# Kernel optimization log

Measured on AMD Instinct MI355X. Metric: run time of the kernel, lower is better.

Reference implementation:

```python
import jax, jax.numpy as jnp
import numpy as np

EPS = 1e-12

def sage_layer(x, src, dst, Wl, Wr, b, n_nodes):
    # mean aggregation of source-node features into destination nodes
    msgs = x[src]                                            # [E, F] gather
    s = jax.ops.segment_sum(msgs, dst, num_segments=n_nodes)  # [N, F]
    cnt = jax.ops.segment_sum(jnp.ones((src.shape[0],), x.dtype), dst, num_segments=n_nodes)
    agg = s / jnp.maximum(cnt, 1.0)[:, None]                 # mean; 0 for isolated nodes
    out = agg @ Wl + b + x @ Wr                              # lin_l(agg) + lin_r(x_i)
    norm = jnp.linalg.norm(out, axis=-1, keepdims=True)      # normalize=True -> L2 norm
    return out / jnp.maximum(norm, EPS)


def setup_inputs() -> dict:
    key = jax.random.key(0)
    ks = jax.random.split(key, 8)
    N, E, F = 100000, 1200000, 64
    H1, H2, OUT = 64, 32, 10  # hidden_channels//2, hidden_channels//4, output_dim
    x = jax.random.normal(ks[0], (N, F), dtype=jnp.float32)
    edge_index = jax.random.randint(ks[1], (2, E), 0, N, dtype=jnp.int64)
    def glorot(k, fin, fout):
        lim = np.sqrt(6.0 / (fin + fout)).astype(np.float32)
        return jax.random.uniform(k, (fin, fout), jnp.float32, -lim, lim)
    return {
        "x": x,
        "edge_index": edge_index,
        "W1l": glorot(ks[2], F, H1), "W1r": glorot(ks[3], F, H1), "b1": jnp.zeros((H1,), jnp.float32),
        "W2l": glorot(ks[4], H1, H2), "W2r": glorot(ks[5], H1, H2), "b2": jnp.zeros((H2,), jnp.float32),
        "W3l": glorot(ks[6], H2, OUT), "W3r": glorot(ks[7], H2, OUT), "b3": jnp.zeros((OUT,), jnp.float32),
    }


def reference(x, edge_index, W1l, W1r, b1, W2l, W2r, b2, W3l, W3r, b3):
    n = x.shape[0]
    src, dst = edge_index[0], edge_index[1]
    h = jax.nn.relu(sage_layer(x, src, dst, W1l, W1r, b1, n))
    h = jax.nn.relu(sage_layer(h, src, dst, W2l, W2r, b2, n))
    h = sage_layer(h, src, dst, W3l, W3r, b3, n)
    return jax.nn.log_softmax(h, axis=1)
```

## Files before the change

kernel.cpp:

```cpp
#include <hip/hip_runtime.h>
#include <math.h>


typedef __attribute__((ext_vector_type(8))) short short8;
typedef __attribute__((ext_vector_type(4))) float floatx4;

__device__ __forceinline__ unsigned short f2bf(float f) {
    unsigned u = __float_as_uint(f);
    u += 0x7fffu + ((u >> 16) & 1u);
    return (unsigned short)(u >> 16);
}
__device__ __forceinline__ float blo(unsigned u) { return __uint_as_float(u << 16); }
__device__ __forceinline__ float bhi(unsigned u) { return __uint_as_float(u & 0xffff0000u); }


__global__ __launch_bounds__(256) void hist_kernel(
        const int* __restrict__ ei, int* __restrict__ bh, int E, int NB, int NBKT) {
    __shared__ int lh[256];
    const int tid = threadIdx.x, blk = blockIdx.x;
    if (tid < NBKT) lh[tid] = 0;
    __syncthreads();
    const int base = blk << 12;
#pragma unroll
    for (int i = 0; i < 16; ++i) {
        const int e = base + (i << 8) + tid;
        if (e < E) atomicAdd(&lh[((unsigned)ei[E + e]) >> 9], 1);
    }
    __syncthreads();
    if (tid < NBKT) bh[tid * NB + blk] = lh[tid];
}

__global__ __launch_bounds__(256) void bscan_kernel(
        const int* __restrict__ bh, int* __restrict__ offs, int* __restrict__ btot,
        int NB, int NBKT) {
    const int lane = threadIdx.x & 63;
    const int w = blockIdx.x * 4 + (threadIdx.x >> 6);
    if (w >= NBKT) return;
    int running = 0;
    for (int base = 0; base < NB; base += 64) {
        const int j = base + lane;
        const int v = (j < NB) ? bh[w * NB + j] : 0;
        int incl = v;
#pragma unroll
        for (int off = 1; off < 64; off <<= 1) {
            const int t = __shfl_up(incl, off);
            if (lane >= off) incl += t;
        }
        if (j < NB) offs[w * NB + j] = running + incl - v;
        running += __shfl(incl, 63);
    }
    if (lane == 0) btot[w] = running;
}

__global__ __launch_bounds__(64) void bucketbase_kernel(
        const int* __restrict__ btot, int* __restrict__ bucket_base, int NBKT) {
    const int lane = threadIdx.x;
    int running = 0;
    for (int base = 0; base < NBKT; base += 64) {
        const int j = base + lane;
        const int v = (j < NBKT) ? btot[j] : 0;
        int incl = v;
#pragma unroll
        for (int off = 1; off < 64; off <<= 1) {
            const int t = __shfl_up(incl, off);
            if (lane >= off) incl += t;
        }
        if (j < NBKT) bucket_base[j] = running + incl - v;
        running += __shfl(incl, 63);
    }
    if (lane == 0) bucket_base[NBKT] = running;
}

__global__ __launch_bounds__(256) void scatter_kernel(
        const int* __restrict__ ei, const int* __restrict__ offs,
        const int* __restrict__ bucket_base, unsigned* __restrict__ ebuf,
        int E, int NB, int NBKT) {
    __shared__ int lcur[256];
    const int tid = threadIdx.x, blk = blockIdx.x;
    if (tid < NBKT) lcur[tid] = bucket_base[tid] + offs[tid * NB + blk];
    __syncthreads();
    const int base = blk << 12;
#pragma unroll
    for (int i = 0; i < 16; ++i) {
        const int e = base + (i << 8) + tid;
        if (e < E) {
            const int s = ei[e];
            const unsigned d = (unsigned)ei[E + e];
            const int p = atomicAdd(&lcur[d >> 9], 1);
            ebuf[p] = ((d & 511u) << 17) | (unsigned)s;
        }
    }
}

__global__ __launch_bounds__(512) void bucket_csr_kernel(
        const unsigned* __restrict__ ebuf, const int* __restrict__ bucket_base,
        int* __restrict__ rowptr, int* __restrict__ deg, int* __restrict__ col,
        int N) {
    __shared__ int ldeg[512];
    __shared__ int buf[512];
    __shared__ int lcur[512];
    const int b = blockIdx.x, tid = threadIdx.x;
    const int segbase = bucket_base[b];
    const int L = bucket_base[b + 1] - segbase;
    ldeg[tid] = 0;
    __syncthreads();
    for (int i = tid; i < L; i += 512) atomicAdd(&ldeg[ebuf[segbase + i] >> 17], 1);
    __syncthreads();
    buf[tid] = ldeg[tid];
    __syncthreads();
    for (int off = 1; off < 512; off <<= 1) {
        const int t = (tid >= off) ? buf[tid - off] : 0;
        __syncthreads();
        buf[tid] += t;
        __syncthreads();
    }
    const int excl = buf[tid] - ldeg[tid];
    const int node = (b << 9) + tid;
    if (node < N) { rowptr[node] = segbase + excl; deg[node] = ldeg[tid]; }
    lcur[tid] = excl;
    __syncthreads();
    for (int i = tid; i < L; i += 512) {
        const unsigned p = ebuf[segbase + i];
        const int pos = atomicAdd(&lcur[p >> 17], 1);
        col[segbase + pos] = (int)(p & 0x1FFFFu);
    }
}

template <int K, int F_OUT, int PAD, bool AFP32>
__global__ __launch_bounds__(256) void transform_kernel(
        const void* __restrict__ Ain, const float* __restrict__ Wl,
        const float* __restrict__ Wr, const float* __restrict__ b,
        unsigned short* __restrict__ yl, float* __restrict__ yr, int n) {
    constexpr int KSTEP = K / 32;
    constexpr int NT = PAD / 16;
    const int lane = threadIdx.x & 63;
    const int wid = (blockIdx.x * blockDim.x + threadIdx.x) >> 6;
    const int ntiles = (n + 15) >> 4;
    if (wid >= ntiles) return;
    const int nl = lane & 15, q = lane >> 4;

    short8 Bl[NT][KSTEP], Br[NT][KSTEP];
    float biasv[NT];
#pragma unroll
    for (int t = 0; t < NT; ++t) {
        const int ncol = t * 16 + nl;
        biasv[t] = (ncol < F_OUT) ? b[ncol] : 0.f;
#pragma unroll
        for (int ks = 0; ks < KSTEP; ++ks) {
#pragma unroll
            for (int j = 0; j < 8; ++j) {
                const int k = ks * 32 + q * 8 + j;
                Bl[t][ks][j] = (ncol < F_OUT) ? (short)f2bf(Wl[k * F_OUT + ncol]) : (short)0;
                Br[t][ks][j] = (ncol < F_OUT) ? (short)f2bf(Wr[k * F_OUT + ncol]) : (short)0;
            }
        }
    }

    const int m0 = wid * 16;
    int m = m0 + nl; if (m >= n) m = n - 1;

    short8 a[KSTEP];
#pragma unroll
    for (int ks = 0; ks < KSTEP; ++ks) {
        if (AFP32) {
            const float* p = (const float*)Ain + (size_t)m * K + ks * 32 + q * 8;
#pragma unroll
            for (int j = 0; j < 8; ++j) a[ks][j] = (short)f2bf(p[j]);
        } else {
            union { uint4 u; short8 s; } cvt;
            cvt.u = *(const uint4*)((const unsigned short*)Ain + (size_t)m * K + ks * 32 + q * 8);
            a[ks] = cvt.s;
        }
    }

    floatx4 accl[NT], accr[NT];
#pragma unroll
    for (int t = 0; t < NT; ++t) { accl[t] = {0.f,0.f,0.f,0.f}; accr[t] = {0.f,0.f,0.f,0.f}; }
#pragma unroll
    for (int ks = 0; ks < KSTEP; ++ks) {
#pragma unroll
        for (int t = 0; t < NT; ++t) {
            accl[t] = __builtin_amdgcn_mfma_f32_16x16x32_bf16(a[ks], Bl[t][ks], accl[t], 0, 0, 0);
            accr[t] = __builtin_amdgcn_mfma_f32_16x16x32_bf16(a[ks], Br[t][ks], accr[t], 0, 0, 0);
        }
    }

#pragma unroll
    for (int t = 0; t < NT; ++t) {
        const int ncol = t * 16 + nl;
#pragma unroll
        for (int r = 0; r < 4; ++r) {
            const int node = m0 + q * 4 + r;
            if (node < n) {
                yl[(size_t)node * PAD + ncol] = f2bf(accl[t][r]);
                yr[(size_t)node * PAD + ncol] = accr[t][r] + biasv[t];
            }
        }
    }
}

template <int F, int ACT>
__global__ __launch_bounds__(256) void agg_kernel(
        const unsigned short* __restrict__ yl, const float* __restrict__ yr,
        const int* __restrict__ rowptr, const int* __restrict__ degv,
        const int* __restrict__ col,
        unsigned short* __restrict__ hout, float* __restrict__ fout, int n) {
    constexpr int G = F / 8;
    constexpr int NPW = 64 / G;
    const int lane = threadIdx.x & 63;
    const int wid = (blockIdx.x * blockDim.x + threadIdx.x) >> 6;
    const int g = lane / G, c = lane % G;
    const int node = wid * NPW + g;
    if (node >= n) return;

    const int beg = rowptr[node];
    const int dg  = degv[node];
    const unsigned short* base = yl + c * 8;

    float a0=0.f,a1=0.f,a2=0.f,a3=0.f,a4=0.f,a5=0.f,a6=0.f,a7=0.f;
    int i = 0;
    for (; i + 2 <= dg; i += 2) {
        const int n0 = col[beg + i], n1 = col[beg + i + 1];
        const uint4 t0 = *(const uint4*)(base + (size_t)n0 * F);
        const uint4 t1 = *(const uint4*)(base + (size_t)n1 * F);
        a0 += blo(t0.x) + blo(t1.x); a1 += bhi(t0.x) + bhi(t1.x);
        a2 += blo(t0.y) + blo(t1.y); a3 += bhi(t0.y) + bhi(t1.y);
        a4 += blo(t0.z) + blo(t1.z); a5 += bhi(t0.z) + bhi(t1.z);
        a6 += blo(t0.w) + blo(t1.w); a7 += bhi(t0.w) + bhi(t1.w);
    }
    if (i < dg) {
        const uint4 t0 = *(const uint4*)(base + (size_t)col[beg + i] * F);
        a0 += blo(t0.x); a1 += bhi(t0.x); a2 += blo(t0.y); a3 += bhi(t0.y);
        a4 += blo(t0.z); a5 += bhi(t0.z); a6 += blo(t0.w); a7 += bhi(t0.w);
    }
    const float inv = (dg > 0) ? 1.f / (float)dg : 0.f;

    const floatx4* yp = (const floatx4*)(yr + (size_t)node * F + c * 8);
    const floatx4 r0 = yp[0], r1 = yp[1];
    float o[8];
    o[0] = a0*inv + r0.x; o[1] = a1*inv + r0.y; o[2] = a2*inv + r0.z; o[3] = a3*inv + r0.w;
    o[4] = a4*inv + r1.x; o[5] = a5*inv + r1.y; o[6] = a6*inv + r1.z; o[7] = a7*inv + r1.w;

    float ss = 0.f;
#pragma unroll
    for (int j = 0; j < 8; ++j) ss += o[j] * o[j];
#pragma unroll
    for (int off = 1; off < G; off <<= 1) ss += __shfl_xor(ss, off);
    const float scale = 1.f / fmaxf(sqrtf(ss), 1e-12f);

    if (ACT == 1) {
        uint4 u;
        float h[8];
#pragma unroll
        for (int j = 0; j < 8; ++j) h[j] = fmaxf(o[j] * scale, 0.f);
        u.x = (unsigned)f2bf(h[0]) | ((unsigned)f2bf(h[1]) << 16);
        u.y = (unsigned)f2bf(h[2]) | ((unsigned)f2bf(h[3]) << 16);
        u.z = (unsigned)f2bf(h[4]) | ((unsigned)f2bf(h[5]) << 16);
        u.w = (unsigned)f2bf(h[6]) | ((unsigned)f2bf(h[7]) << 16);
        *(uint4*)(hout + (size_t)node * F + c * 8) = u;
    } else {
#pragma unroll
        for (int j = 0; j < 8; ++j) o[j] *= scale;
        const int cbase = c * 8;
        float m = -INFINITY;
#pragma unroll
        for (int j = 0; j < 8; ++j) if (cbase + j < 10) m = fmaxf(m, o[j]);
        m = fmaxf(m, __shfl_xor(m, 1));
        float s = 0.f;
#pragma unroll
        for (int j = 0; j < 8; ++j) if (cbase + j < 10) s += __expf(o[j] - m);
        s += __shfl_xor(s, 1);
        const float ls = logf(s);
#pragma unroll
        for (int j = 0; j < 8; ++j)
            if (cbase + j < 10) fout[(size_t)node * 10 + cbase + j] = o[j] - m - ls;
    }
}

extern "C" void kernel_launch(void* const* d_in, const int* in_sizes, int n_in,
                              void* d_out, int out_size, void* d_ws, size_t ws_size,
                              hipStream_t stream) {
    const float* x   = (const float*)d_in[0];
    const int*   ei  = (const int*)d_in[1];
    const float* W1l = (const float*)d_in[2];
    const float* W1r = (const float*)d_in[3];
    const float* b1  = (const float*)d_in[4];
    const float* W2l = (const float*)d_in[5];
    const float* W2r = (const float*)d_in[6];
    const float* b2  = (const float*)d_in[7];
    const float* W3l = (const float*)d_in[8];
    const float* W3r = (const float*)d_in[9];
    const float* b3  = (const float*)d_in[10];
    float*       out = (float*)d_out;

    const int N = in_sizes[0] / 64;
    const int E = in_sizes[1] / 2;
    const int NBKT = (N + 511) >> 9;
    const int NB   = (E + 4095) >> 12;

    auto align16 = [](size_t v) { return (v + 15) & ~(size_t)15; };
    char* ws = (char*)d_ws;
    size_t off = 0;
    int* rowptr  = (int*)(ws + off); off = align16(off + (size_t)N * 4);
    int* deg     = (int*)(ws + off); off = align16(off + (size_t)N * 4);
    int* colidx  = (int*)(ws + off); off = align16(off + (size_t)E * 4);
    unsigned* ebuf = (unsigned*)(ws + off); off = align16(off + (size_t)E * 4);
    int* bh      = (int*)(ws + off); off = align16(off + (size_t)NBKT * NB * 4);
    int* offsb   = (int*)(ws + off); off = align16(off + (size_t)NBKT * NB * 4);
    int* btot    = (int*)(ws + off); off = align16(off + (size_t)NBKT * 4);
    int* bbase   = (int*)(ws + off); off = align16(off + (size_t)(NBKT + 1) * 4);
    unsigned short* y1l = (unsigned short*)(ws + off); off = align16(off + (size_t)N * 64 * 2);
    float*          y1r = (float*)(ws + off);          off = align16(off + (size_t)N * 64 * 4);
    unsigned short* h1  = (unsigned short*)(ws + off); off = align16(off + (size_t)N * 64 * 2);
    unsigned short* y2l = (unsigned short*)(ws + off); off = align16(off + (size_t)N * 32 * 2);
    float*          y2r = (float*)(ws + off);          off = align16(off + (size_t)N * 32 * 4);
    unsigned short* h2  = (unsigned short*)(ws + off); off = align16(off + (size_t)N * 32 * 2);
    unsigned short* y3l = (unsigned short*)(ws + off); off = align16(off + (size_t)N * 16 * 2);
    float*          y3r = (float*)(ws + off);          off = align16(off + (size_t)N * 16 * 4);
    (void)ws_size; (void)n_in; (void)out_size;

    hist_kernel<<<NB, 256, 0, stream>>>(ei, bh, E, NB, NBKT);
    bscan_kernel<<<(NBKT + 3) / 4, 256, 0, stream>>>(bh, offsb, btot, NB, NBKT);
    bucketbase_kernel<<<1, 64, 0, stream>>>(btot, bbase, NBKT);
    scatter_kernel<<<NB, 256, 0, stream>>>(ei, offsb, bbase, ebuf, E, NB, NBKT);
    bucket_csr_kernel<<<NBKT, 512, 0, stream>>>(ebuf, bbase, rowptr, deg, colidx, N);

    const int ntiles = (N + 15) / 16;
    const int tblocks = (ntiles * 64 + 255) / 256;

    transform_kernel<64, 64, 64, true><<<tblocks, 256, 0, stream>>>(x, W1l, W1r, b1, y1l, y1r, N);
    agg_kernel<64, 1><<<(N + 31) / 32, 256, 0, stream>>>(y1l, y1r, rowptr, deg, colidx, h1, nullptr, N);
    transform_kernel<64, 32, 32, false><<<tblocks, 256, 0, stream>>>(h1, W2l, W2r, b2, y2l, y2r, N);
    agg_kernel<32, 1><<<(N + 63) / 64, 256, 0, stream>>>(y2l, y2r, rowptr, deg, colidx, h2, nullptr, N);
    transform_kernel<32, 10, 16, false><<<tblocks, 256, 0, stream>>>(h2, W3l, W3r, b3, y3l, y3r, N);
    agg_kernel<16, 2><<<(N + 127) / 128, 256, 0, stream>>>(y3l, y3r, rowptr, deg, colidx, nullptr, out, N);
}
```

Baseline: 248.8 us.

## Sort nodes by degree for load-balanced aggregation and unroll gather by four

```diff
diff --git a/kernel.cpp b/kernel.cpp
--- a/kernel.cpp
+++ b/kernel.cpp
@@ -123,6 +123,40 @@
         const unsigned p = ebuf[segbase + i];
         const int pos = atomicAdd(&lcur[p >> 17], 1);
         col[segbase + pos] = (int)(p & 0x1FFFFu);
+    }
+}
+
+__global__ __launch_bounds__(512) void deg_hist_kernel(
+        const int* __restrict__ deg, int* __restrict__ dh, int N, int NDB) {
+    __shared__ int lh[512];
+    const int tid = threadIdx.x, blk = blockIdx.x;
+    lh[tid] = 0;
+    __syncthreads();
+    const int base = blk << 12;
+#pragma unroll
+    for (int i = 0; i < 8; ++i) {
+        const int node = base + (i << 9) + tid;
+        if (node < N) atomicAdd(&lh[min(deg[node], 511)], 1);
+    }
+    __syncthreads();
+    dh[tid * NDB + blk] = lh[tid];
+}
+
+__global__ __launch_bounds__(512) void deg_scatter_kernel(
+        const int* __restrict__ deg, const int* __restrict__ doffs,
+        const int* __restrict__ degbase, int* __restrict__ perm, int N, int NDB) {
+    __shared__ int lcur[512];
+    const int tid = threadIdx.x, blk = blockIdx.x;
+    lcur[tid] = degbase[tid] + doffs[tid * NDB + blk];
+    __syncthreads();
+    const int base = blk << 12;
+#pragma unroll
+    for (int i = 0; i < 8; ++i) {
+        const int node = base + (i << 9) + tid;
+        if (node < N) {
+            const int pos = atomicAdd(&lcur[min(deg[node], 511)], 1);
+            perm[pos] = node;
+        }
     }
 }
 
@@ -203,15 +237,16 @@
 __global__ __launch_bounds__(256) void agg_kernel(
         const unsigned short* __restrict__ yl, const float* __restrict__ yr,
         const int* __restrict__ rowptr, const int* __restrict__ degv,
-        const int* __restrict__ col,
+        const int* __restrict__ col, const int* __restrict__ perm,
         unsigned short* __restrict__ hout, float* __restrict__ fout, int n) {
     constexpr int G = F / 8;
     constexpr int NPW = 64 / G;
     const int lane = threadIdx.x & 63;
     const int wid = (blockIdx.x * blockDim.x + threadIdx.x) >> 6;
     const int g = lane / G, c = lane % G;
-    const int node = wid * NPW + g;
-    if (node >= n) return;
+    const int idx = wid * NPW + g;
+    if (idx >= n) return;
+    const int node = perm[idx];
 
     const int beg = rowptr[node];
     const int dg  = degv[node];
@@ -219,16 +254,23 @@
 
     float a0=0.f,a1=0.f,a2=0.f,a3=0.f,a4=0.f,a5=0.f,a6=0.f,a7=0.f;
     int i = 0;
-    for (; i + 2 <= dg; i += 2) {
+    for (; i + 4 <= dg; i += 4) {
         const int n0 = col[beg + i], n1 = col[beg + i + 1];
+        const int n2 = col[beg + i + 2], n3 = col[beg + i + 3];
         const uint4 t0 = *(const uint4*)(base + (size_t)n0 * F);
         const uint4 t1 = *(const uint4*)(base + (size_t)n1 * F);
-        a0 += blo(t0.x) + blo(t1.x); a1 += bhi(t0.x) + bhi(t1.x);
-        a2 += blo(t0.y) + blo(t1.y); a3 += bhi(t0.y) + bhi(t1.y);
-        a4 += blo(t0.z) + blo(t1.z); a5 += bhi(t0.z) + bhi(t1.z);
-        a6 += blo(t0.w) + blo(t1.w); a7 += bhi(t0.w) + bhi(t1.w);
-    }
-    if (i < dg) {
+        const uint4 t2 = *(const uint4*)(base + (size_t)n2 * F);
+        const uint4 t3 = *(const uint4*)(base + (size_t)n3 * F);
+        a0 += blo(t0.x) + blo(t1.x) + blo(t2.x) + blo(t3.x);
+        a1 += bhi(t0.x) + bhi(t1.x) + bhi(t2.x) + bhi(t3.x);
+        a2 += blo(t0.y) + blo(t1.y) + blo(t2.y) + blo(t3.y);
+        a3 += bhi(t0.y) + bhi(t1.y) + bhi(t2.y) + bhi(t3.y);
+        a4 += blo(t0.z) + blo(t1.z) + blo(t2.z) + blo(t3.z);
+        a5 += bhi(t0.z) + bhi(t1.z) + bhi(t2.z) + bhi(t3.z);
+        a6 += blo(t0.w) + blo(t1.w) + blo(t2.w) + blo(t3.w);
+        a7 += bhi(t0.w) + bhi(t1.w) + bhi(t2.w) + bhi(t3.w);
+    }
+    for (; i < dg; ++i) {
         const uint4 t0 = *(const uint4*)(base + (size_t)col[beg + i] * F);
         a0 += blo(t0.x); a1 += bhi(t0.x); a2 += blo(t0.y); a3 += bhi(t0.y);
         a4 += blo(t0.z); a5 += bhi(t0.z); a6 += blo(t0.w); a7 += bhi(t0.w);
@@ -297,18 +339,24 @@
     const int E = in_sizes[1] / 2;
     const int NBKT = (N + 511) >> 9;
     const int NB   = (E + 4095) >> 12;
+    const int NDB  = (N + 4095) >> 12;
 
     auto align16 = [](size_t v) { return (v + 15) & ~(size_t)15; };
     char* ws = (char*)d_ws;
     size_t off = 0;
     int* rowptr  = (int*)(ws + off); off = align16(off + (size_t)N * 4);
     int* deg     = (int*)(ws + off); off = align16(off + (size_t)N * 4);
+    int* perm    = (int*)(ws + off); off = align16(off + (size_t)N * 4);
     int* colidx  = (int*)(ws + off); off = align16(off + (size_t)E * 4);
     unsigned* ebuf = (unsigned*)(ws + off); off = align16(off + (size_t)E * 4);
     int* bh      = (int*)(ws + off); off = align16(off + (size_t)NBKT * NB * 4);
     int* offsb   = (int*)(ws + off); off = align16(off + (size_t)NBKT * NB * 4);
     int* btot    = (int*)(ws + off); off = align16(off + (size_t)NBKT * 4);
     int* bbase   = (int*)(ws + off); off = align16(off + (size_t)(NBKT + 1) * 4);
+    int* dh      = (int*)(ws + off); off = align16(off + (size_t)512 * NDB * 4);
+    int* doffs   = (int*)(ws + off); off = align16(off + (size_t)512 * NDB * 4);
+    int* dtot    = (int*)(ws + off); off = align16(off + (size_t)512 * 4);
+    int* degbase = (int*)(ws + off); off = align16(off + (size_t)513 * 4);
     unsigned short* y1l = (unsigned short*)(ws + off); off = align16(off + (size_t)N * 64 * 2);
     float*          y1r = (float*)(ws + off);          off = align16(off + (size_t)N * 64 * 4);
     unsigned short* h1  = (unsigned short*)(ws + off); off = align16(off + (size_t)N * 64 * 2);
@@ -325,13 +373,18 @@
     scatter_kernel<<<NB, 256, 0, stream>>>(ei, offsb, bbase, ebuf, E, NB, NBKT);
     bucket_csr_kernel<<<NBKT, 512, 0, stream>>>(ebuf, bbase, rowptr, deg, colidx, N);
 
+    deg_hist_kernel<<<NDB, 512, 0, stream>>>(deg, dh, N, NDB);
+    bscan_kernel<<<(512 + 3) / 4, 256, 0, stream>>>(dh, doffs, dtot, NDB, 512);
+    bucketbase_kernel<<<1, 64, 0, stream>>>(dtot, degbase, 512);
+    deg_scatter_kernel<<<NDB, 512, 0, stream>>>(deg, doffs, degbase, perm, N, NDB);
+
     const int ntiles = (N + 15) / 16;
     const int tblocks = (ntiles * 64 + 255) / 256;
 
     transform_kernel<64, 64, 64, true><<<tblocks, 256, 0, stream>>>(x, W1l, W1r, b1, y1l, y1r, N);
-    agg_kernel<64, 1><<<(N + 31) / 32, 256, 0, stream>>>(y1l, y1r, rowptr, deg, colidx, h1, nullptr, N);
+    agg_kernel<64, 1><<<(N + 31) / 32, 256, 0, stream>>>(y1l, y1r, rowptr, deg, colidx, perm, h1, nullptr, N);
     transform_kernel<64, 32, 32, false><<<tblocks, 256, 0, stream>>>(h1, W2l, W2r, b2, y2l, y2r, N);
-    agg_kernel<32, 1><<<(N + 63) / 64, 256, 0, stream>>>(y2l, y2r, rowptr, deg, colidx, h2, nullptr, N);
+    agg_kernel<32, 1><<<(N + 63) / 64, 256, 0, stream>>>(y2l, y2r, rowptr, deg, colidx, perm, h2, nullptr, N);
     transform_kernel<32, 10, 16, false><<<tblocks, 256, 0, stream>>>(h2, W3l, W3r, b3, y3l, y3r, N);
-    agg_kernel<16, 2><<<(N + 127) / 128, 256, 0, stream>>>(y3l, y3r, rowptr, deg, colidx, nullptr, out, N);
-}
+    agg_kernel<16, 2><<<(N + 127) / 128, 256, 0, stream>>>(y3l, y3r, rowptr, deg, colidx, perm, nullptr, out, N);
+}
```

Measured after the change: 281.7 us. 1.13x slower.
